# Kernel tuning notes

Measured on AMD Instinct MI355X. Metric: run time of the kernel, lower is better.

Reference implementation:

```python
import math
import jax, jax.numpy as jnp
import numpy as np

B, S, E, H = 2, 2048, 1024, 16
Dh = E // H  # 64
ROPE_BASE = 10000.0


def setup_inputs() -> dict:
    key = jax.random.key(0)
    ks = jax.random.split(key, 7)
    f32 = jnp.float32
    return {
        "q": jax.random.normal(ks[0], (B, S, E), dtype=f32),
        "k": jax.random.normal(ks[1], (B, S, E), dtype=f32),
        "v": jax.random.normal(ks[2], (B, S, E), dtype=f32),
        # nn.Linear weights stored torch-style as [out_features, in_features]
        "W_q": jax.random.normal(ks[3], (E, E), dtype=f32) * 0.02,
        "W_k": jax.random.normal(ks[4], (E, E), dtype=f32) * 0.02,
        "W_v": jax.random.normal(ks[5], (E, E), dtype=f32) * 0.02,
        "W_o": jax.random.normal(ks[6], (E, E), dtype=f32) * 0.02,
    }


def _rope(x):
    # x: [B, H, S, Dh]; interleaved-pair rotary embedding along the seq axis.
    d = x.shape[-1]
    pos = jnp.arange(x.shape[2], dtype=x.dtype)
    inv_freq = 1.0 / (ROPE_BASE ** (jnp.arange(0, d, 2, dtype=x.dtype) / d))
    ang = pos[:, None] * inv_freq            # [S, Dh//2]
    cos, sin = jnp.cos(ang), jnp.sin(ang)    # broadcast over [B, H]
    xe, xo = x[..., 0::2], x[..., 1::2]      # even/odd interleaved pairs
    out = jnp.stack([xe * cos - xo * sin, xo * cos + xe * sin], axis=-1)
    return out.reshape(x.shape)


def reference(q, k, v, W_q, W_k, W_v, W_o):
    b, s, e = q.shape
    scale = 1.0 / math.sqrt(e)  # NOTE: 1/sqrt(hidden_dim), not head_dim (faithful)
    # project and split heads: [B, H, S, Dh]
    qh = (q @ W_q.T).reshape(b, s, H, Dh).transpose(0, 2, 1, 3)
    kh = (k @ W_k.T).reshape(b, s, H, Dh).transpose(0, 2, 1, 3)
    vh = (v @ W_v.T).reshape(b, s, H, Dh).transpose(0, 2, 1, 3)
    qh = _rope(qh)
    kh = _rope(kh)
    scores = jnp.einsum('bhsd,bhtd->bhst', qh, kh) * scale
    # Faithful quirk: the original sets causal_mask[0,0] = False, which zeroes
    # the ENTIRE [S,S] mask (dims 0,1 are singletons) -> masked_fill is a no-op.
    probs = jax.nn.softmax(scores, axis=-1)
    out = jnp.einsum('bhst,bhtd->bhsd', probs, vh)
    out = out.transpose(0, 2, 1, 3).reshape(b, s, e)
    return out @ W_o.T
```

## Files before the change

### kernel.cpp

```cpp
#include <hip/hip_runtime.h>
#include <math.h>

#define Bsz 2
#define Ssz 2048
#define Esz 1024
#define Hn  16
#define Dd  64
#define PADC 72

typedef unsigned short ushort_t;
typedef short bf16x8 __attribute__((ext_vector_type(8)));
typedef float f32x4 __attribute__((ext_vector_type(4)));

#define GLD16(g, l) __builtin_amdgcn_global_load_lds(                        \
    (const __attribute__((address_space(1))) unsigned int*)(g),              \
    (__attribute__((address_space(3))) unsigned int*)(l), 16, 0, 0)

#define KF 0.045084220027780106f

__global__ __launch_bounds__(256) void rope_table_kernel(float* tc, float* ts)
{
    const int idx = blockIdx.x * 256 + threadIdx.x;
    const int s = idx >> 5, p = idx & 31;
    const double c = 9.210340371976184257 / 32.0;
    const double inv = exp(-c * (double)p);
    double sn, cs;
    sincos((double)s * inv, &sn, &cs);
    tc[idx] = (float)cs;
    ts[idx] = (float)sn;
}

__device__ inline ushort_t bf16_rn(float x)
{
    unsigned u = __float_as_uint(x);
    return (ushort_t)((u + 0x7FFFu + ((u >> 16) & 1u)) >> 16);
}

__global__ __launch_bounds__(256) void cvt_kernel(
    const float* s0, const float* s1, const float* s2, const float* s3,
    const float* s4, const float* s5, const float* s6,
    ushort_t* d0, ushort_t* d1, ushort_t* d2, ushort_t* d3,
    ushort_t* d4, ushort_t* d5, ushort_t* d6, int n_big, int n_small)
{
    const float* s; ushort_t* d;
    switch (blockIdx.z) {
        case 0: s = s0; d = d0; break;
        case 1: s = s1; d = d1; break;
        case 2: s = s2; d = d2; break;
        case 3: s = s3; d = d3; break;
        case 4: s = s4; d = d4; break;
        case 5: s = s5; d = d5; break;
        default: s = s6; d = d6; break;
    }
    const int n = (blockIdx.z < 3) ? n_big : n_small;
    const int i = (blockIdx.x * 256 + threadIdx.x) * 4;
    if (i >= n) return;
    float4 v = *(const float4*)(s + i);
    ushort4 o;
    o.x = bf16_rn(v.x); o.y = bf16_rn(v.y);
    o.z = bf16_rn(v.z); o.w = bf16_rn(v.w);
    *(ushort4*)(d + i) = o;
}

__global__ __launch_bounds__(256) void proj_gemm_kernel(
    const ushort_t* __restrict__ Aq, const ushort_t* __restrict__ Ak,
    const ushort_t* __restrict__ Av,
    const ushort_t* __restrict__ Wq, const ushort_t* __restrict__ Wk,
    const ushort_t* __restrict__ Wv,
    ushort_t* __restrict__ Yq, ushort_t* __restrict__ Yk,
    ushort_t* __restrict__ Yv,
    const float* __restrict__ tc, const float* __restrict__ ts)
{
    const int z = blockIdx.z;
    const ushort_t* Ag = (z == 0) ? Aq : (z == 1) ? Ak : Av;
    const ushort_t* Wg = (z == 0) ? Wq : (z == 1) ? Wk : Wv;
    ushort_t*       Yg = (z == 0) ? Yq : (z == 1) ? Yk : Yv;

    __shared__ __align__(16) ushort_t sA[128 * 32];
    __shared__ __align__(16) ushort_t sB[128 * 32];

    const int t    = threadIdx.x;
    const int lane = t & 63;
    const int w    = t >> 6;
    const int wm   = (w & 1) * 64;
    const int wn   = (w >> 1) * 64;
    const int fr   = lane & 15;
    const int g    = lane >> 4;
    const int kq   = g * 8;
    const int n0   = blockIdx.x * 128;
    const int m0   = blockIdx.y * 128;

    const ushort_t* pA = Ag + (size_t)(m0 + (t >> 2)) * 1024 + (t & 3) * 8;
    const ushort_t* pB = Wg + (size_t)(n0 + (t >> 2)) * 1024 + (t & 3) * 8;

    f32x4 acc[4][4];
#pragma unroll
    for (int mi = 0; mi < 4; ++mi)
#pragma unroll
        for (int ni = 0; ni < 4; ++ni) acc[mi][ni] = (f32x4)0.f;

    for (int k0 = 0; k0 < 1024; k0 += 32) {
        GLD16(pA + k0,             &sA[t * 8]);
        GLD16(pA + k0 + 64 * 1024, &sA[2048 + t * 8]);
        GLD16(pB + k0,             &sB[t * 8]);
        GLD16(pB + k0 + 64 * 1024, &sB[2048 + t * 8]);
        __syncthreads();

        bf16x8 a[4], b[4];
#pragma unroll
        for (int mi = 0; mi < 4; ++mi)
            a[mi] = *(const bf16x8*)&sA[(wm + mi * 16 + fr) * 32 + kq];
#pragma unroll
        for (int ni = 0; ni < 4; ++ni)
            b[ni] = *(const bf16x8*)&sB[(wn + ni * 16 + fr) * 32 + kq];
#pragma unroll
        for (int mi = 0; mi < 4; ++mi)
#pragma unroll
            for (int ni = 0; ni < 4; ++ni)
                acc[mi][ni] = __builtin_amdgcn_mfma_f32_16x16x32_bf16(
                    a[mi], b[ni], acc[mi][ni], 0, 0, 0);
        __syncthreads();
    }

#pragma unroll
    for (int mi = 0; mi < 4; ++mi)
#pragma unroll
        for (int ni = 0; ni < 4; ++ni) {
            const int col   = n0 + wn + ni * 16 + fr;
            const int rbase = m0 + wm + mi * 16 + g * 4;
            const int hh = col >> 6, d = col & 63, pi = d >> 1;
#pragma unroll
            for (int rg = 0; rg < 4; ++rg) {
                const int srow = rbase + rg;
                const int b_ = srow >> 11, s = srow & (Ssz - 1);
                float v  = acc[mi][ni][rg];
                float pt = __shfl_xor(v, 1, 64);
                float o  = v;
                if (z < 2) {
                    const float cs = tc[s * 32 + pi];
                    const float sn = ts[s * 32 + pi];
                    o = (d & 1) ? fmaf(v, cs, pt * sn)
                                : fmaf(v, cs, -pt * sn);
                    if (z == 0) o *= KF;
                }
                const size_t idx = (z == 2)
                    ? (((size_t)(b_ * Hn + hh)) * Dd + d) * Ssz + s
                    : (((size_t)(b_ * Hn + hh)) * Ssz + s) * Dd + d;
                Yg[idx] = bf16_rn(o);
            }
        }
}

__global__ __launch_bounds__(256) void attn_kernel(
    const ushort_t* __restrict__ Qb, const ushort_t* __restrict__ Kb,
    const ushort_t* __restrict__ Vtb, ushort_t* __restrict__ Ob)
{
    __shared__ __align__(16) ushort_t sK[64 * PADC];
    __shared__ __align__(16) ushort_t sV[64 * PADC];
    __shared__ __align__(16) ushort_t sP[128 * PADC];

    const int t    = threadIdx.x;
    const int lane = t & 63;
    const int w    = t >> 6;
    const int fr   = lane & 15;
    const int g    = lane >> 4;
    const int kq   = g * 8;
    const int bh   = blockIdx.y;
    const int q0   = blockIdx.x * 128;

    const int frh = fr >> 3;
    const int frl = fr & 7;
    const int fq  = (fr >> 2) & 3;

    int scolP[4], krdP[2];
#pragma unroll
    for (int nt = 0; nt < 4; ++nt)
        scolP[nt] = (((nt * 2 + frh) ^ g) << 3) + frl;
#pragma unroll
    for (int ks = 0; ks < 2; ++ks)
        krdP[ks] = ((4 * ks + g) ^ fq) << 3;

    bf16x8 qa[2][2];
#pragma unroll
    for (int mt = 0; mt < 2; ++mt) {
        const size_t qbase = ((size_t)bh * Ssz + q0 + w * 32 + mt * 16 + fr) * Dd;
        qa[mt][0] = *(const bf16x8*)(Qb + qbase + kq);
        qa[mt][1] = *(const bf16x8*)(Qb + qbase + 32 + kq);
    }

    float lp[2][4];
    f32x4 Oacc[2][4];
#pragma unroll
    for (int mt = 0; mt < 2; ++mt) {
#pragma unroll
        for (int rg = 0; rg < 4; ++rg) lp[mt][rg] = 0.f;
#pragma unroll
        for (int dt = 0; dt < 4; ++dt) Oacc[mt][dt] = (f32x4)0.f;
    }

    const int srow = t >> 3;
    const int scol = (t & 7) * 8;
    const size_t kgb = (size_t)bh * Ssz * Dd;
    const size_t vgb = (size_t)bh * Dd * Ssz;

    for (int kv0 = 0; kv0 < Ssz; kv0 += 64) {
#pragma unroll
        for (int rr = 0; rr < 2; ++rr) {
            const int row = srow + rr * 32;
            *(uint4*)&sK[row * PADC + scol] =
                *(const uint4*)(Kb + kgb + (size_t)(kv0 + row) * Dd + scol);
            *(uint4*)&sV[row * PADC + scol] =
                *(const uint4*)(Vtb + vgb + (size_t)row * Ssz + kv0 + scol);
        }
        __syncthreads();

        f32x4 S[2][4];
#pragma unroll
        for (int mt = 0; mt < 2; ++mt)
#pragma unroll
            for (int nt = 0; nt < 4; ++nt) S[mt][nt] = (f32x4)0.f;
#pragma unroll
        for (int ks = 0; ks < 2; ++ks)
#pragma unroll
            for (int nt = 0; nt < 4; ++nt) {
                bf16x8 kfrag = *(const bf16x8*)&sK[(nt * 16 + fr) * PADC + ks * 32 + kq];
#pragma unroll
                for (int mt = 0; mt < 2; ++mt)
                    S[mt][nt] = __builtin_amdgcn_mfma_f32_16x16x32_bf16(
                        qa[mt][ks], kfrag, S[mt][nt], 0, 0, 0);
            }

#pragma unroll
        for (int mt = 0; mt < 2; ++mt)
#pragma unroll
            for (int nt = 0; nt < 4; ++nt)
#pragma unroll
                for (int rg = 0; rg < 4; ++rg) {
                    const float p = exp2f(S[mt][nt][rg]);
                    lp[mt][rg] += p;
                    sP[(w * 32 + mt * 16 + g * 4 + rg) * PADC + scolP[nt]] =
                        (ushort_t)(__float_as_uint(p) >> 16);
                }
        __syncthreads();

#pragma unroll
        for (int ks = 0; ks < 2; ++ks) {
            bf16x8 pa[2];
#pragma unroll
            for (int mt = 0; mt < 2; ++mt)
                pa[mt] = *(const bf16x8*)&sP[(w * 32 + mt * 16 + fr) * PADC + krdP[ks]];
#pragma unroll
            for (int dt = 0; dt < 4; ++dt) {
                bf16x8 vfrag = *(const bf16x8*)&sV[(dt * 16 + fr) * PADC + ks * 32 + kq];
#pragma unroll
                for (int mt = 0; mt < 2; ++mt)
                    Oacc[mt][dt] = __builtin_amdgcn_mfma_f32_16x16x32_bf16(
                        pa[mt], vfrag, Oacc[mt][dt], 0, 0, 0);
            }
        }
        __syncthreads();
    }

#pragma unroll
    for (int mt = 0; mt < 2; ++mt)
#pragma unroll
        for (int rg = 0; rg < 4; ++rg) {
#pragma unroll
            for (int mk = 1; mk <= 8; mk <<= 1)
                lp[mt][rg] += __shfl_xor(lp[mt][rg], mk, 64);
        }

    const int b = bh >> 4, h = bh & 15;
#pragma unroll
    for (int mt = 0; mt < 2; ++mt)
#pragma unroll
        for (int rg = 0; rg < 4; ++rg) {
            const int s = q0 + w * 32 + mt * 16 + g * 4 + rg;
            const float inv = 1.f / lp[mt][rg];
#pragma unroll
            for (int dt = 0; dt < 4; ++dt) {
                const float o = Oacc[mt][dt][rg] * inv;
                Ob[((size_t)(b * Ssz + s)) * Esz + h * Dd + dt * 16 + fr] = bf16_rn(o);
            }
        }
}

__global__ __launch_bounds__(256) void final_gemm_kernel(
    const ushort_t* __restrict__ Ag, const ushort_t* __restrict__ Bg,
    float* __restrict__ Yf)
{
    __shared__ __align__(16) ushort_t sA[128 * 32];
    __shared__ __align__(16) ushort_t sB[128 * 32];

    const int t    = threadIdx.x;
    const int lane = t & 63;
    const int w    = t >> 6;
    const int wm   = (w & 1) * 64;
    const int wn   = (w >> 1) * 64;
    const int fr   = lane & 15;
    const int g    = lane >> 4;
    const int kq   = g * 8;
    const int n0   = blockIdx.x * 128;
    const int m0   = blockIdx.y * 128;

    const ushort_t* pA = Ag + (size_t)(m0 + (t >> 2)) * 1024 + (t & 3) * 8;
    const ushort_t* pB = Bg + (size_t)(n0 + (t >> 2)) * 1024 + (t & 3) * 8;

    f32x4 acc[4][4];
#pragma unroll
    for (int mi = 0; mi < 4; ++mi)
#pragma unroll
        for (int ni = 0; ni < 4; ++ni) acc[mi][ni] = (f32x4)0.f;

    for (int k0 = 0; k0 < 1024; k0 += 32) {
        GLD16(pA + k0,             &sA[t * 8]);
        GLD16(pA + k0 + 64 * 1024, &sA[2048 + t * 8]);
        GLD16(pB + k0,             &sB[t * 8]);
        GLD16(pB + k0 + 64 * 1024, &sB[2048 + t * 8]);
        __syncthreads();

        bf16x8 a[4], b[4];
#pragma unroll
        for (int mi = 0; mi < 4; ++mi)
            a[mi] = *(const bf16x8*)&sA[(wm + mi * 16 + fr) * 32 + kq];
#pragma unroll
        for (int ni = 0; ni < 4; ++ni)
            b[ni] = *(const bf16x8*)&sB[(wn + ni * 16 + fr) * 32 + kq];
#pragma unroll
        for (int mi = 0; mi < 4; ++mi)
#pragma unroll
            for (int ni = 0; ni < 4; ++ni)
                acc[mi][ni] = __builtin_amdgcn_mfma_f32_16x16x32_bf16(
                    a[mi], b[ni], acc[mi][ni], 0, 0, 0);
        __syncthreads();
    }

#pragma unroll
    for (int mi = 0; mi < 4; ++mi)
#pragma unroll
        for (int ni = 0; ni < 4; ++ni) {
            const int col   = n0 + wn + ni * 16 + fr;
            const int rbase = m0 + wm + mi * 16 + g * 4;
#pragma unroll
            for (int rg = 0; rg < 4; ++rg)
                Yf[(size_t)(rbase + rg) * 1024 + col] = acc[mi][ni][rg];
        }
}

extern "C" void kernel_launch(void* const* d_in, const int* in_sizes, int n_in,
                              void* d_out, int out_size, void* d_ws, size_t ws_size,
                              hipStream_t stream)
{
    (void)in_sizes; (void)n_in; (void)out_size; (void)ws_size;
    const float* q   = (const float*)d_in[0];
    const float* k   = (const float*)d_in[1];
    const float* v   = (const float*)d_in[2];
    const float* W_q = (const float*)d_in[3];
    const float* W_k = (const float*)d_in[4];
    const float* W_v = (const float*)d_in[5];
    const float* W_o = (const float*)d_in[6];
    float* out = (float*)d_out;

    const size_t NQ = (size_t)Bsz * Ssz * Esz;
    const size_t NW = (size_t)Esz * Esz;

    float* ws = (float*)d_ws;
    float* tc = ws;
    float* ts = ws + 65536;

    ushort_t* us  = (ushort_t*)(ws + 131072);
    ushort_t* qb  = us;
    ushort_t* kb  = qb + NQ;
    ushort_t* vb  = kb + NQ;
    ushort_t* wqb = vb + NQ;
    ushort_t* wkb = wqb + NW;
    ushort_t* wvb = wkb + NW;
    ushort_t* wob = wvb + NW;
    ushort_t* pq  = wob + NW;
    ushort_t* pk  = pq + NQ;
    ushort_t* pv  = pk + NQ;
    ushort_t* ob  = pv + NQ;

    dim3 blk(256);

    rope_table_kernel<<<dim3(256), blk, 0, stream>>>(tc, ts);

    cvt_kernel<<<dim3(4096, 1, 7), blk, 0, stream>>>(
        q, k, v, W_q, W_k, W_v, W_o,
        qb, kb, vb, wqb, wkb, wvb, wob, (int)NQ, (int)NW);

    proj_gemm_kernel<<<dim3(Esz / 128, (Bsz * Ssz) / 128, 3), blk, 0, stream>>>(
        qb, kb, vb, wqb, wkb, wvb, pq, pk, pv, tc, ts);

    attn_kernel<<<dim3(Ssz / 128, Bsz * Hn), blk, 0, stream>>>(pq, pk, pv, ob);

    final_gemm_kernel<<<dim3(Esz / 128, (Bsz * Ssz) / 128), blk, 0, stream>>>(
        ob, wob, out);
}
```

Measured before the change: 312.1 us.

## Stage GEMM epilogues through LDS, keep attention P in registers, fuse rope table

The projection and output GEMM epilogues now write through an LDS tile, so global stores become coalesced 16-byte vector stores instead of scattered 2- or 4-byte writes, including the transposed V layout. Attention computes S transposed so the exponentiated probabilities feed a 16x16x16 MFMA straight from registers, which removes the sP shared buffer and one barrier per KV tile. The rope table kernel is folded into the conversion kernel as an extra grid slice to save a launch. In exchange the kernels use more LDS, which may lower occupancy, the PV product uses the smaller K=16 MFMA, and the row sums now need extra shuffles.

```diff
diff --git a/kernel.cpp b/kernel.cpp
--- a/kernel.cpp
+++ b/kernel.cpp
@@ -7,9 +7,12 @@
 #define Hn  16
 #define Dd  64
 #define PADC 72
+#define TP   136
+#define FP   68
 
 typedef unsigned short ushort_t;
 typedef short bf16x8 __attribute__((ext_vector_type(8)));
+typedef short bf16x4 __attribute__((ext_vector_type(4)));
 typedef float f32x4 __attribute__((ext_vector_type(4)));
 
 #define GLD16(g, l) __builtin_amdgcn_global_load_lds(                        \
@@ -18,17 +21,8 @@
 
 #define KF 0.045084220027780106f
 
-__global__ __launch_bounds__(256) void rope_table_kernel(float* tc, float* ts)
-{
-    const int idx = blockIdx.x * 256 + threadIdx.x;
-    const int s = idx >> 5, p = idx & 31;
-    const double c = 9.210340371976184257 / 32.0;
-    const double inv = exp(-c * (double)p);
-    double sn, cs;
-    sincos((double)s * inv, &sn, &cs);
-    tc[idx] = (float)cs;
-    ts[idx] = (float)sn;
-}
+#define MFMA32(a, b, c) __builtin_amdgcn_mfma_f32_16x16x32_bf16((a), (b), (c), 0, 0, 0)
+#define MFMA16(a, b, c) __builtin_amdgcn_mfma_f32_16x16x16bf16_1k((a), (b), (c), 0, 0, 0)
 
 __device__ inline ushort_t bf16_rn(float x)
 {
@@ -40,8 +34,22 @@
     const float* s0, const float* s1, const float* s2, const float* s3,
     const float* s4, const float* s5, const float* s6,
     ushort_t* d0, ushort_t* d1, ushort_t* d2, ushort_t* d3,
-    ushort_t* d4, ushort_t* d5, ushort_t* d6, int n_big, int n_small)
-{
+    ushort_t* d4, ushort_t* d5, ushort_t* d6,
+    float* tc, float* ts, int n_big, int n_small)
+{
+    if (blockIdx.z == 7) {
+        const int idx = blockIdx.x * 256 + threadIdx.x;
+        if (idx < Ssz * 32) {
+            const int s = idx >> 5, p = idx & 31;
+            const double c = 9.210340371976184257 / 32.0;
+            const double inv = exp(-c * (double)p);
+            double sn, cs;
+            sincos((double)s * inv, &sn, &cs);
+            tc[idx] = (float)cs;
+            ts[idx] = (float)sn;
+        }
+        return;
+    }
     const float* s; ushort_t* d;
     switch (blockIdx.z) {
         case 0: s = s0; d = d0; break;
@@ -78,6 +86,7 @@
 
     __shared__ __align__(16) ushort_t sA[128 * 32];
     __shared__ __align__(16) ushort_t sB[128 * 32];
+    __shared__ __align__(16) ushort_t Tb[128 * TP];
 
     const int t    = threadIdx.x;
     const int lane = t & 63;
@@ -117,8 +126,7 @@
         for (int mi = 0; mi < 4; ++mi)
 #pragma unroll
             for (int ni = 0; ni < 4; ++ni)
-                acc[mi][ni] = __builtin_amdgcn_mfma_f32_16x16x32_bf16(
-                    a[mi], b[ni], acc[mi][ni], 0, 0, 0);
+                acc[mi][ni] = MFMA32(a[mi], b[ni], acc[mi][ni]);
         __syncthreads();
     }
 
@@ -126,13 +134,13 @@
     for (int mi = 0; mi < 4; ++mi)
 #pragma unroll
         for (int ni = 0; ni < 4; ++ni) {
-            const int col   = n0 + wn + ni * 16 + fr;
-            const int rbase = m0 + wm + mi * 16 + g * 4;
-            const int hh = col >> 6, d = col & 63, pi = d >> 1;
+            const int col = wn + ni * 16 + fr;
+            const int d   = (n0 + col) & 63;
+            const int pi  = d >> 1;
 #pragma unroll
             for (int rg = 0; rg < 4; ++rg) {
-                const int srow = rbase + rg;
-                const int b_ = srow >> 11, s = srow & (Ssz - 1);
+                const int row = wm + mi * 16 + g * 4 + rg;
+                const int s   = (m0 + row) & (Ssz - 1);
                 float v  = acc[mi][ni][rg];
                 float pt = __shfl_xor(v, 1, 64);
                 float o  = v;
@@ -143,12 +151,45 @@
                                 : fmaf(v, cs, -pt * sn);
                     if (z == 0) o *= KF;
                 }
-                const size_t idx = (z == 2)
-                    ? (((size_t)(b_ * Hn + hh)) * Dd + d) * Ssz + s
-                    : (((size_t)(b_ * Hn + hh)) * Ssz + s) * Dd + d;
-                Yg[idx] = bf16_rn(o);
-            }
-        }
+                Tb[row * TP + col] = bf16_rn(o);
+            }
+        }
+    __syncthreads();
+
+    if (z < 2) {
+        const int row = t >> 1;
+        const int m   = m0 + row;
+        const int b   = m >> 11, s = m & (Ssz - 1);
+#pragma unroll
+        for (int i = 0; i < 8; ++i) {
+            const int ic = (t & 1) * 8 + i;
+            uint4 val = *(const uint4*)&Tb[row * TP + ic * 8];
+            const int hh = (n0 >> 6) + (ic >> 3);
+            const int d  = (ic & 7) * 8;
+            *(uint4*)&Yg[(((size_t)(b * Hn + hh)) * Ssz + s) * Dd + d] = val;
+        }
+    } else {
+        const int col = t >> 1;
+        const int hh  = (n0 >> 6) + (col >> 6);
+        const int d   = col & 63;
+        const int b   = m0 >> 11;
+        const int sg  = (m0 & (Ssz - 1)) + (t & 1) * 64;
+        const size_t base = (((size_t)(b * Hn + hh)) * Dd + d) * Ssz + sg;
+#pragma unroll
+        for (int jj = 0; jj < 8; ++jj) {
+            uint4 val;
+            unsigned vv[4];
+#pragma unroll
+            for (int qd = 0; qd < 4; ++qd) {
+                const int r0 = (t & 1) * 64 + jj * 8 + qd * 2;
+                const unsigned lo = Tb[(r0 + 0) * TP + col];
+                const unsigned hi = Tb[(r0 + 1) * TP + col];
+                vv[qd] = lo | (hi << 16);
+            }
+            val.x = vv[0]; val.y = vv[1]; val.z = vv[2]; val.w = vv[3];
+            *(uint4*)&Yg[base + jj * 8] = val;
+        }
+    }
 }
 
 __global__ __launch_bounds__(256) void attn_kernel(
@@ -157,7 +198,6 @@
 {
     __shared__ __align__(16) ushort_t sK[64 * PADC];
     __shared__ __align__(16) ushort_t sV[64 * PADC];
-    __shared__ __align__(16) ushort_t sP[128 * PADC];
 
     const int t    = threadIdx.x;
     const int lane = t & 63;
@@ -168,18 +208,6 @@
     const int bh   = blockIdx.y;
     const int q0   = blockIdx.x * 128;
 
-    const int frh = fr >> 3;
-    const int frl = fr & 7;
-    const int fq  = (fr >> 2) & 3;
-
-    int scolP[4], krdP[2];
-#pragma unroll
-    for (int nt = 0; nt < 4; ++nt)
-        scolP[nt] = (((nt * 2 + frh) ^ g) << 3) + frl;
-#pragma unroll
-    for (int ks = 0; ks < 2; ++ks)
-        krdP[ks] = ((4 * ks + g) ^ fq) << 3;
-
     bf16x8 qa[2][2];
 #pragma unroll
     for (int mt = 0; mt < 2; ++mt) {
@@ -188,15 +216,12 @@
         qa[mt][1] = *(const bf16x8*)(Qb + qbase + 32 + kq);
     }
 
-    float lp[2][4];
+    float lp[2] = {0.f, 0.f};
     f32x4 Oacc[2][4];
 #pragma unroll
-    for (int mt = 0; mt < 2; ++mt) {
-#pragma unroll
-        for (int rg = 0; rg < 4; ++rg) lp[mt][rg] = 0.f;
+    for (int mt = 0; mt < 2; ++mt)
 #pragma unroll
         for (int dt = 0; dt < 4; ++dt) Oacc[mt][dt] = (f32x4)0.f;
-    }
 
     const int srow = t >> 3;
     const int scol = (t & 7) * 8;
@@ -214,11 +239,11 @@
         }
         __syncthreads();
 
-        f32x4 S[2][4];
+        f32x4 St[2][4];
 #pragma unroll
         for (int mt = 0; mt < 2; ++mt)
 #pragma unroll
-            for (int nt = 0; nt < 4; ++nt) S[mt][nt] = (f32x4)0.f;
+            for (int nt = 0; nt < 4; ++nt) St[mt][nt] = (f32x4)0.f;
 #pragma unroll
         for (int ks = 0; ks < 2; ++ks)
 #pragma unroll
@@ -226,57 +251,51 @@
                 bf16x8 kfrag = *(const bf16x8*)&sK[(nt * 16 + fr) * PADC + ks * 32 + kq];
 #pragma unroll
                 for (int mt = 0; mt < 2; ++mt)
-                    S[mt][nt] = __builtin_amdgcn_mfma_f32_16x16x32_bf16(
-                        qa[mt][ks], kfrag, S[mt][nt], 0, 0, 0);
-            }
-
+                    St[mt][nt] = MFMA32(kfrag, qa[mt][ks], St[mt][nt]);
+            }
+
+        bf16x4 pf[2][4];
 #pragma unroll
         for (int mt = 0; mt < 2; ++mt)
 #pragma unroll
-            for (int nt = 0; nt < 4; ++nt)
-#pragma unroll
-                for (int rg = 0; rg < 4; ++rg) {
-                    const float p = exp2f(S[mt][nt][rg]);
-                    lp[mt][rg] += p;
-                    sP[(w * 32 + mt * 16 + g * 4 + rg) * PADC + scolP[nt]] =
-                        (ushort_t)(__float_as_uint(p) >> 16);
-                }
-        __syncthreads();
-
-#pragma unroll
-        for (int ks = 0; ks < 2; ++ks) {
-            bf16x8 pa[2];
-#pragma unroll
-            for (int mt = 0; mt < 2; ++mt)
-                pa[mt] = *(const bf16x8*)&sP[(w * 32 + mt * 16 + fr) * PADC + krdP[ks]];
+            for (int nt = 0; nt < 4; ++nt) {
+                const float p0 = exp2f(St[mt][nt][0]);
+                const float p1 = exp2f(St[mt][nt][1]);
+                const float p2 = exp2f(St[mt][nt][2]);
+                const float p3 = exp2f(St[mt][nt][3]);
+                lp[mt] += (p0 + p1) + (p2 + p3);
+                union { unsigned u[2]; bf16x4 s; } pk;
+                pk.u[0] = (__float_as_uint(p0) >> 16) | (__float_as_uint(p1) & 0xFFFF0000u);
+                pk.u[1] = (__float_as_uint(p2) >> 16) | (__float_as_uint(p3) & 0xFFFF0000u);
+                pf[mt][nt] = pk.s;
+            }
+
+#pragma unroll
+        for (int nt = 0; nt < 4; ++nt)
 #pragma unroll
             for (int dt = 0; dt < 4; ++dt) {
-                bf16x8 vfrag = *(const bf16x8*)&sV[(dt * 16 + fr) * PADC + ks * 32 + kq];
+                bf16x4 vfrag = *(const bf16x4*)&sV[(dt * 16 + fr) * PADC + nt * 16 + g * 4];
 #pragma unroll
                 for (int mt = 0; mt < 2; ++mt)
-                    Oacc[mt][dt] = __builtin_amdgcn_mfma_f32_16x16x32_bf16(
-                        pa[mt], vfrag, Oacc[mt][dt], 0, 0, 0);
-            }
-        }
-        __syncthreads();
-    }
-
+                    Oacc[mt][dt] = MFMA16(pf[mt][nt], vfrag, Oacc[mt][dt]);
+            }
+        __syncthreads();
+    }
+
+#pragma unroll
+    for (int mt = 0; mt < 2; ++mt) {
+        lp[mt] += __shfl_xor(lp[mt], 16, 64);
+        lp[mt] += __shfl_xor(lp[mt], 32, 64);
+    }
+
+    const int b = bh >> 4, h = bh & 15;
 #pragma unroll
     for (int mt = 0; mt < 2; ++mt)
 #pragma unroll
         for (int rg = 0; rg < 4; ++rg) {
-#pragma unroll
-            for (int mk = 1; mk <= 8; mk <<= 1)
-                lp[mt][rg] += __shfl_xor(lp[mt][rg], mk, 64);
-        }
-
-    const int b = bh >> 4, h = bh & 15;
-#pragma unroll
-    for (int mt = 0; mt < 2; ++mt)
-#pragma unroll
-        for (int rg = 0; rg < 4; ++rg) {
+            const float lv  = __shfl(lp[mt], (lane & 48) + g * 4 + rg, 64);
+            const float inv = 1.f / lv;
             const int s = q0 + w * 32 + mt * 16 + g * 4 + rg;
-            const float inv = 1.f / lp[mt][rg];
 #pragma unroll
             for (int dt = 0; dt < 4; ++dt) {
                 const float o = Oacc[mt][dt][rg] * inv;
@@ -291,6 +310,7 @@
 {
     __shared__ __align__(16) ushort_t sA[128 * 32];
     __shared__ __align__(16) ushort_t sB[128 * 32];
+    __shared__ __align__(16) float Tf[128 * FP];
 
     const int t    = threadIdx.x;
     const int lane = t & 63;
@@ -330,21 +350,32 @@
         for (int mi = 0; mi < 4; ++mi)
 #pragma unroll
             for (int ni = 0; ni < 4; ++ni)
-                acc[mi][ni] = __builtin_amdgcn_mfma_f32_16x16x32_bf16(
-                    a[mi], b[ni], acc[mi][ni], 0, 0, 0);
-        __syncthreads();
-    }
-
-#pragma unroll
-    for (int mi = 0; mi < 4; ++mi)
-#pragma unroll
-        for (int ni = 0; ni < 4; ++ni) {
-            const int col   = n0 + wn + ni * 16 + fr;
-            const int rbase = m0 + wm + mi * 16 + g * 4;
-#pragma unroll
-            for (int rg = 0; rg < 4; ++rg)
-                Yf[(size_t)(rbase + rg) * 1024 + col] = acc[mi][ni][rg];
-        }
+                acc[mi][ni] = MFMA32(a[mi], b[ni], acc[mi][ni]);
+        __syncthreads();
+    }
+
+#pragma unroll
+    for (int hf = 0; hf < 2; ++hf) {
+        if ((w >> 1) == hf) {
+#pragma unroll
+            for (int mi = 0; mi < 4; ++mi)
+#pragma unroll
+                for (int ni = 0; ni < 4; ++ni) {
+                    const int col = ni * 16 + fr;
+#pragma unroll
+                    for (int rg = 0; rg < 4; ++rg)
+                        Tf[(wm + mi * 16 + g * 4 + rg) * FP + col] = acc[mi][ni][rg];
+                }
+        }
+        __syncthreads();
+        const int row = t >> 1;
+        float* dst = Yf + (size_t)(m0 + row) * 1024 + n0 + hf * 64 + (t & 1) * 32;
+        const float* src = &Tf[row * FP + (t & 1) * 32];
+#pragma unroll
+        for (int i = 0; i < 8; ++i)
+            *(float4*)(dst + i * 4) = *(const float4*)(src + i * 4);
+        __syncthreads();
+    }
 }
 
 extern "C" void kernel_launch(void* const* d_in, const int* in_sizes, int n_in,
@@ -383,11 +414,9 @@
 
     dim3 blk(256);
 
-    rope_table_kernel<<<dim3(256), blk, 0, stream>>>(tc, ts);
-
-    cvt_kernel<<<dim3(4096, 1, 7), blk, 0, stream>>>(
+    cvt_kernel<<<dim3(4096, 1, 8), blk, 0, stream>>>(
         q, k, v, W_q, W_k, W_v, W_o,
-        qb, kb, vb, wqb, wkb, wvb, wob, (int)NQ, (int)NW);
+        qb, kb, vb, wqb, wkb, wvb, wob, tc, ts, (int)NQ, (int)NW);
 
     proj_gemm_kernel<<<dim3(Esz / 128, (Bsz * Ssz) / 128, 3), blk, 0, stream>>>(
         qb, kb, vb, wqb, wkb, wvb, pq, pk, pv, tc, ts);
```

Result: faster. 295.9 us (-5.2%).
